# Performance work log

Measured on AMD Instinct MI355X. Metric: run time of the kernel, lower is better.

Reference implementation:

```python
import jax, jax.numpy as jnp
import numpy as np

C = 64            # x_channel (d_model)
D = 2 * C         # d_inner (expand=2)
N = C // 2        # d_state
K = 4             # scan directions
R = -(-C // 16)   # dt_rank = ceil(d_model/16)
Bsz, H, W = 2, 48, 48
EPS = 1e-5


def setup_inputs() -> dict:
    key = jax.random.key(0)
    ks = jax.random.split(key, 8)
    g = lambda k, shp, s: jax.random.normal(k, shp, dtype=jnp.float32) * s
    return {
        "fufea1": g(ks[0], (Bsz, C, H, W), 1.0),
        "ln_g": jnp.ones((C,), jnp.float32),
        "ln_b": jnp.zeros((C,), jnp.float32),
        "in_proj_w": g(ks[1], (2 * D, C), C ** -0.5),
        "conv_w": g(ks[2], (D, 1, 3, 3), 1.0 / 3.0),   # depthwise 3x3
        "conv_b": g(ks[3], (D,), 0.02),
        "x_proj_w": g(ks[4], (K, R + 2 * N, D), D ** -0.5),
        "dt_w": g(ks[5], (K, D, R), R ** -0.5),
        "dt_b": g(ks[6], (K, D), 0.1),
        "A_logs": jnp.log(jnp.tile(jnp.arange(1, N + 1, dtype=jnp.float32), (K, D, 1))),  # S4D-real init
        "Ds": jnp.ones((K, D), jnp.float32),
        "out_ln_g": jnp.ones((D,), jnp.float32),
        "out_ln_b": jnp.zeros((D,), jnp.float32),
        "out_proj_w": g(ks[7], (C, D), D ** -0.5),
    }


def _layernorm(x, g, b):
    mu = x.mean(-1, keepdims=True)
    var = ((x - mu) ** 2).mean(-1, keepdims=True)
    return (x - mu) * jax.lax.rsqrt(var + EPS) * g + b


def reference(fufea1, ln_g, ln_b, in_proj_w, conv_w, conv_b, x_proj_w,
              dt_w, dt_b, A_logs, Ds, out_ln_g, out_ln_b, out_proj_w):
    B, Cc, Hh, Ww = fufea1.shape
    L = Hh * Ww
    # pre-LN (over channels, channels-last)
    xn = _layernorm(fufea1.transpose(0, 2, 3, 1), ln_g, ln_b)          # (B,H,W,C)
    # SS2D: in_proj -> split x,z
    xz = xn @ in_proj_w.T                                               # (B,H,W,2D)
    x, z = jnp.split(xz, 2, axis=-1)
    x = x.transpose(0, 3, 1, 2)                                         # (B,D,H,W)
    x = jax.lax.conv_general_dilated(x, conv_w, (1, 1), "SAME",
                                     feature_group_count=D,
                                     dimension_numbers=("NCHW", "OIHW", "NCHW"))
    x = jax.nn.silu(x + conv_b[None, :, None, None])
    # 4-direction sequences: row-major, col-major, and their reverses
    x_hw = x.reshape(B, D, L)
    x_wh = x.transpose(0, 1, 3, 2).reshape(B, D, L)
    xs = jnp.stack([x_hw, x_wh], axis=1)                                # (B,2,D,L)
    xs = jnp.concatenate([xs, jnp.flip(xs, axis=-1)], axis=1)           # (B,K,D,L)
    # per-direction projections of dt, B, C
    x_dbl = jnp.einsum("bkdl,kcd->bkcl", xs, x_proj_w)
    dts, Bs, Cs = jnp.split(x_dbl, [R, R + N], axis=2)                  # (B,K,R,L),(B,K,N,L),(B,K,N,L)
    dts = jnp.einsum("bkrl,kdr->bkdl", dts, dt_w)
    delta = jax.nn.softplus(dts + dt_b[None, :, :, None])               # (B,K,D,L)
    A = -jnp.exp(A_logs)                                                # (K,D,N)
    # selective scan over L; carry h: (B,K,D,N)
    u_l = xs.transpose(3, 0, 1, 2)                                      # (L,B,K,D)
    dt_l = delta.transpose(3, 0, 1, 2)
    B_l = Bs.transpose(3, 0, 1, 2)                                      # (L,B,K,N)
    C_l = Cs.transpose(3, 0, 1, 2)

    def step(h, inp):
        u_t, d_t, b_t, c_t = inp
        dA = jnp.exp(d_t[..., None] * A)                                # (B,K,D,N)
        h = dA * h + (d_t * u_t)[..., None] * b_t[:, :, None, :]
        y = jnp.einsum("bkdn,bkn->bkd", h, c_t)
        return h, y

    h0 = jnp.zeros((B, K, D, N), xs.dtype)
    _, ys = jax.lax.scan(step, h0, (u_l, dt_l, B_l, C_l))               # ys: (L,B,K,D)
    out_y = ys.transpose(1, 2, 3, 0) + Ds[None, :, :, None] * xs        # (B,K,D,L)
    # merge the 4 directions back to row-major hw order
    inv_y = jnp.flip(out_y[:, 2:4], axis=-1)                            # (B,2,D,L)
    wh = lambda t: t.reshape(B, D, Ww, Hh).transpose(0, 1, 3, 2).reshape(B, D, L)
    y = out_y[:, 0] + inv_y[:, 0] + wh(out_y[:, 1]) + wh(inv_y[:, 1])   # (B,D,L)
    y = y.transpose(0, 2, 1).reshape(B, Hh, Ww, D)
    y = _layernorm(y, out_ln_g, out_ln_b) * jax.nn.silu(z)
    out = (y @ out_proj_w.T).transpose(0, 3, 1, 2) + fufea1             # residual add
    return out
```

## Files before the change

kernel.cpp:

```cpp
#include <hip/hip_runtime.h>

#define Cc 64
#define Dd 128
#define Nn 32
#define Kk 4
#define Rr 4
#define Bb 2
#define Hh 48
#define Ww 48
#define Ll 2304
#define EPSf 1e-5f
#define LCc 144

#if __has_builtin(__builtin_amdgcn_exp2f)
#define EXP2F __builtin_amdgcn_exp2f
#else
#define EXP2F exp2f
#endif

__device__ __forceinline__ float wsum64(float v) {
  v += __shfl_xor(v, 32);
  v += __shfl_xor(v, 16);
  v += __shfl_xor(v, 8);
  v += __shfl_xor(v, 4);
  v += __shfl_xor(v, 2);
  v += __shfl_xor(v, 1);
  return v;
}

__device__ __forceinline__ float hmax32(float v) {
  v = fmaxf(v, __shfl_xor(v, 1));
  v = fmaxf(v, __shfl_xor(v, 2));
  v = fmaxf(v, __shfl_xor(v, 4));
  v = fmaxf(v, __shfl_xor(v, 8));
  v = fmaxf(v, __shfl_xor(v, 16));
  return v;
}

__global__ __launch_bounds__(256) void k1_ln_inproj(
    const float* __restrict__ x, const float* __restrict__ g,
    const float* __restrict__ bta, const float* __restrict__ Wp,
    float* __restrict__ xin, float* __restrict__ zb)
{
  __shared__ float xS[16][65];
  __shared__ float xnS[16][64];
  const int tid = threadIdx.x;
  const int wv = tid >> 6, lane = tid & 63;
  const int pbase = blockIdx.x * 16;
  const int b = pbase / Ll;
  const int lbase = pbase % Ll;
  {
    const int c = tid >> 2, li0 = (tid & 3) * 4;
    const float4 v4 = *(const float4*)&x[(b * Cc + c) * Ll + lbase + li0];
    xS[li0 + 0][c] = v4.x;
    xS[li0 + 1][c] = v4.y;
    xS[li0 + 2][c] = v4.z;
    xS[li0 + 3][c] = v4.w;
  }
  __syncthreads();
  const float gv = g[lane], bv = bta[lane];
  for (int pi = 0; pi < 4; ++pi) {
    const int p = wv * 4 + pi;
    const float v = xS[p][lane];
    const float mu = wsum64(v) * (1.0f / 64.0f);
    const float dv = v - mu;
    const float var = wsum64(dv * dv) * (1.0f / 64.0f);
    const float rs = rsqrtf(var + EPSf);
    xnS[p][lane] = dv * rs * gv + bv;
  }
  __syncthreads();
  float acc[4][4];
  #pragma unroll
  for (int pi = 0; pi < 4; ++pi)
    #pragma unroll
    for (int m = 0; m < 4; ++m) acc[pi][m] = 0.f;
  const float4* W4 = (const float4*)Wp;
  #pragma unroll 4
  for (int c4 = 0; c4 < 16; ++c4) {
    float4 xn4[4];
    #pragma unroll
    for (int pi = 0; pi < 4; ++pi)
      xn4[pi] = ((const float4*)xnS[wv * 4 + pi])[c4];
    #pragma unroll
    for (int m = 0; m < 4; ++m) {
      const float4 w4 = W4[(lane + 64 * m) * 16 + c4];
      #pragma unroll
      for (int pi = 0; pi < 4; ++pi)
        acc[pi][m] += xn4[pi].x * w4.x + xn4[pi].y * w4.y +
                      xn4[pi].z * w4.z + xn4[pi].w * w4.w;
    }
  }
  #pragma unroll
  for (int pi = 0; pi < 4; ++pi) {
    const int l = lbase + wv * 4 + pi;
    const size_t base = (size_t)(b * Ll + l) * Dd;
    xin[base + lane]      = acc[pi][0];
    xin[base + lane + 64] = acc[pi][1];
    zb[base + lane]       = acc[pi][2];
    zb[base + lane + 64]  = acc[pi][3];
  }
}

__global__ __launch_bounds__(512) void k3_proj(
    const float* __restrict__ xin, const float* __restrict__ cw,
    const float* __restrict__ cb, const float* __restrict__ xpw,
    const float* __restrict__ dtw, const float* __restrict__ dtb,
    float* __restrict__ xc, float2* __restrict__ dd2,
    float* __restrict__ Bm, float* __restrict__ Cm)
{
  __shared__ float xinS[128][31];
  __shared__ float xvS[8][132];
  __shared__ float dtsS[8][16];
  const int t = threadIdx.x;
  const int pb = blockIdx.x * 8;
  const int b = pb / Ll;
  const int lb = pb % Ll;
  const int h0 = lb / Ww, w0 = lb % Ww;
  for (int i = t; i < 3840; i += 512) {
    const int d = i & 127, j = i >> 7;
    const int r = j / 10, c = j % 10;
    const int hh = h0 + r - 1, ww = w0 + c - 1;
    float v = 0.f;
    if (hh >= 0 && hh < Hh && ww >= 0 && ww < Ww)
      v = xin[((size_t)(b * Ll) + hh * Ww + ww) * Dd + d];
    xinS[d][j] = v;
  }
  __syncthreads();
  for (int i = t; i < 1024; i += 512) {
    const int pi = i >> 7, d = i & 127;
    float acc = cb[d];
    #pragma unroll
    for (int r = 0; r < 3; ++r)
      #pragma unroll
      for (int c = 0; c < 3; ++c)
        acc += xinS[d][r * 10 + pi + c] * cw[d * 9 + r * 3 + c];
    const float sig = 1.0f / (1.0f + __expf(-acc));
    xvS[pi][d] = acc * sig;
  }
  __syncthreads();
  if (t < 272) {
    const int k = t / 68, c = t % 68;
    const size_t bkL = (size_t)(b * Kk + k) * Ll;
    float acc[8];
    #pragma unroll
    for (int pi = 0; pi < 8; ++pi) acc[pi] = 0.f;
    const float4* w4p = (const float4*)(xpw + (k * 68 + c) * 128);
    for (int d4 = 0; d4 < 32; ++d4) {
      const float4 w4 = w4p[d4];
      #pragma unroll
      for (int pi = 0; pi < 8; ++pi) {
        const float4 x4 = ((const float4*)xvS[pi])[d4];
        acc[pi] += x4.x * w4.x + x4.y * w4.y + x4.z * w4.z + x4.w * w4.w;
      }
    }
    #pragma unroll
    for (int pi = 0; pi < 8; ++pi) {
      const int l0 = lb + pi;
      const int h = l0 / Ww, w = l0 % Ww;
      int lk;
      if      (k == 0) lk = l0;
      else if (k == 1) lk = w * Hh + h;
      else if (k == 2) lk = Ll - 1 - l0;
      else             lk = Ll - 1 - (w * Hh + h);
      if (c < Rr)            dtsS[pi][k * 4 + c] = acc[pi];
      else if (c < Rr + Nn)  Bm[(bkL + lk) * Nn + (c - Rr)] = acc[pi];
      else                   Cm[(bkL + lk) * Nn + (c - Rr - Nn)] = acc[pi];
    }
  } else {
    for (int i = t - 272; i < 1024; i += 240) {
      const int pi = i >> 7, d = i & 127;
      xc[((size_t)(b * Ll) + lb + pi) * Dd + d] = xvS[pi][d];
    }
  }
  __syncthreads();
  {
    const int k = t >> 7, dd = t & 127;
    const float4 dw = *(const float4*)&dtw[(k * Dd + dd) * 4];
    const float biasv = dtb[k * Dd + dd];
    float2* drow = dd2 + ((size_t)((b * Kk + k) * Dd) + dd) * Ll;
    float2 buf[8];
    #pragma unroll
    for (int pi = 0; pi < 8; ++pi) {
      const float a = biasv
          + dtsS[pi][k * 4 + 0] * dw.x + dtsS[pi][k * 4 + 1] * dw.y
          + dtsS[pi][k * 4 + 2] * dw.z + dtsS[pi][k * 4 + 3] * dw.w;
      const float sp = (a > 20.f) ? a : log1pf(__expf(a));
      buf[pi] = make_float2(sp, sp * xvS[pi][dd]);
    }
    if (k == 0) {
      float4* f4 = (float4*)(drow + lb);
      #pragma unroll
      for (int j = 0; j < 4; ++j)
        f4[j] = make_float4(buf[2 * j].x, buf[2 * j].y, buf[2 * j + 1].x, buf[2 * j + 1].y);
    } else if (k == 2) {
      float4* f4 = (float4*)(drow + (Ll - 8 - lb));
      #pragma unroll
      for (int j = 0; j < 4; ++j)
        f4[j] = make_float4(buf[7 - 2 * j].x, buf[7 - 2 * j].y, buf[6 - 2 * j].x, buf[6 - 2 * j].y);
    } else {
      #pragma unroll
      for (int pi = 0; pi < 8; ++pi) {
        const int l0 = lb + pi;
        const int h = l0 / Ww, w = l0 % Ww;
        int lk = w * Hh + h;
        if (k == 3) lk = Ll - 1 - lk;
        drow[lk] = buf[pi];
      }
    }
  }
}

__global__ __launch_bounds__(512) void k4_scan(
    const float2* __restrict__ dd2, const float* __restrict__ Bm,
    const float* __restrict__ Cm, const float* __restrict__ Alogs,
    float* __restrict__ ys)
{
  __shared__ float hendS[16][32];
  __shared__ float carryS[16][32];
  __shared__ float sumDS[16];
  __shared__ float cmaxS[16];
  __shared__ float pS[16][8][36];
  const int tid = threadIdx.x;
  const int s = tid >> 5, n = tid & 31;
  const int blk = blockIdx.x;
  const int bk = blk & 7;
  const int d = blk >> 3;
  const int b = bk >> 2, k = bk & 3;
  const float An = -__expf(Alogs[(k * Dd + d) * Nn + n]);
  const float AnE = An * 1.44269504f;
  const size_t bkL = (size_t)(b * Kk + k) * Ll;
  const float2* dP = dd2 + ((size_t)((b * Kk + k) * Dd) + d) * Ll;
  const float* bP = Bm + bkL * Nn + n;
  const float* cP = Cm + bkL * Nn + n;
  const int lbeg = s * LCc;
  float* yP = ys + ((size_t)((b * Kk + k) * Dd) + d) * Ll + lbeg;
  const int rrow = n & 7, qtr = n >> 3;

  float h = 0.f, sumD = 0.f, cmx = 0.f;
  {
    const float4* q4 = (const float4*)(dP + lbeg);
    const float* bl = bP + (size_t)lbeg * Nn;
    const float* cl = cP + (size_t)lbeg * Nn;
    float4 qa = q4[0], qb = q4[1];
    float b0 = bl[0], b1 = bl[Nn], b2 = bl[2 * Nn], b3 = bl[3 * Nn];
    float c0 = cl[0], c1 = cl[Nn], c2 = cl[2 * Nn], c3 = cl[3 * Nn];
    for (int t8 = 0; t8 < LCc / 8; ++t8) {
      #pragma unroll
      for (int half = 0; half < 2; ++half) {
        q4 += 2; bl += 4 * Nn; cl += 4 * Nn;
        const float4 qa_n = q4[0], qb_n = q4[1];
        const float b0n = bl[0], b1n = bl[Nn], b2n = bl[2 * Nn], b3n = bl[3 * Nn];
        const float c0n = cl[0], c1n = cl[Nn], c2n = cl[2 * Nn], c3n = cl[3 * Nn];
        h = EXP2F(qa.x * AnE) * h + qa.y * b0; pS[s][half * 4 + 0][n] = h * c0;
        h = EXP2F(qa.z * AnE) * h + qa.w * b1; pS[s][half * 4 + 1][n] = h * c1;
        h = EXP2F(qb.x * AnE) * h + qb.y * b2; pS[s][half * 4 + 2][n] = h * c2;
        h = EXP2F(qb.z * AnE) * h + qb.w * b3; pS[s][half * 4 + 3][n] = h * c3;
        sumD += (qa.x + qa.z) + (qb.x + qb.z);
        cmx = fmaxf(cmx, fmaxf(fmaxf(fabsf(c0), fabsf(c1)),
                               fmaxf(fabsf(c2), fabsf(c3))));
        qa = qa_n; qb = qb_n; b0 = b0n; b1 = b1n; b2 = b2n; b3 = b3n;
        c0 = c0n; c1 = c1n; c2 = c2n; c3 = c3n;
      }
      const float4 a4 = *(const float4*)&pS[s][rrow][qtr * 8];
      const float4 d4v = *(const float4*)&pS[s][rrow][qtr * 8 + 4];
      float sum = ((a4.x + a4.y) + (a4.z + a4.w)) + ((d4v.x + d4v.y) + (d4v.z + d4v.w));
      sum += __shfl_xor(sum, 8);
      sum += __shfl_xor(sum, 16);
      if (n < 8) yP[t8 * 8 + n] = sum;
    }
  }
  hendS[s][n] = h;
  const float cmxAll = hmax32(cmx);
  if (n == 0) { sumDS[s] = sumD; cmaxS[s] = cmxAll; }
  __syncthreads();
  if (tid < 32) {
    float carry = 0.f;
    #pragma unroll
    for (int s2 = 0; s2 < 16; ++s2) {
      carryS[s2][tid] = carry;
      carry = EXP2F(AnE * sumDS[s2]) * carry + hendS[s2][tid];
    }
  }
  __syncthreads();
  const float carry = carryS[s][n];
  const float mc = hmax32(fabsf(carry));
  const float AmaxE = hmax32(AnE);
  const float Pstop = log2f(mc * cmaxS[s] * 3.2e6f) / (-AmaxE);
  {
    float hc = carry, P = 0.f;
    const float4* q4 = (const float4*)(dP + lbeg);
    const float* cl = cP + (size_t)lbeg * Nn;
    for (int t8 = 0; t8 < LCc / 8; ++t8) {
      if (!(P < Pstop)) break;
      #pragma unroll
      for (int half = 0; half < 2; ++half) {
        const float4 qa = q4[0], qb = q4[1];
        q4 += 2;
        hc *= EXP2F(qa.x * AnE); pS[s][half * 4 + 0][n] = hc * cl[0];
        hc *= EXP2F(qa.z * AnE); pS[s][half * 4 + 1][n] = hc * cl[Nn];
        hc *= EXP2F(qb.x * AnE); pS[s][half * 4 + 2][n] = hc * cl[2 * Nn];
        hc *= EXP2F(qb.z * AnE); pS[s][half * 4 + 3][n] = hc * cl[3 * Nn];
        P += (qa.x + qa.z) + (qb.x + qb.z);
        cl += 4 * Nn;
      }
      const float4 a4 = *(const float4*)&pS[s][rrow][qtr * 8];
      const float4 d4v = *(const float4*)&pS[s][rrow][qtr * 8 + 4];
      float sum = ((a4.x + a4.y) + (a4.z + a4.w)) + ((d4v.x + d4v.y) + (d4v.z + d4v.w));
      sum += __shfl_xor(sum, 8);
      sum += __shfl_xor(sum, 16);
      if (n < 8) yP[t8 * 8 + n] += sum;
    }
  }
}

__global__ __launch_bounds__(256) void k5_merge(
    const float* __restrict__ ys, const float* __restrict__ zb,
    const float* __restrict__ og, const float* __restrict__ ob,
    const float* __restrict__ Wo, const float* __restrict__ resid,
    const float* __restrict__ xc, const float* __restrict__ DsP,
    float* __restrict__ out)
{
  __shared__ float ysS[4][16][128];
  __shared__ float tS[16][128];
  __shared__ float oS[64][17];
  __shared__ float xcS[16][128];
  const int tid = threadIdx.x;
  const int wv = tid >> 6, lane = tid & 63;
  const int tb = blockIdx.x;
  const int b = tb / 144;
  const int ti = tb % 144;
  const int tr = ti / 12, tc = ti % 12;
  const int h0 = tr * 4, w0 = tc * 4;
  {
    const int p = tid >> 4, qq = tid & 15;
    const int l0 = (h0 + (p >> 2)) * Ww + w0 + (p & 3);
    const float4* src = (const float4*)&xc[((size_t)(b * Ll) + l0) * Dd];
    ((float4*)xcS[p])[qq]      = src[qq];
    ((float4*)xcS[p])[qq + 16] = src[qq + 16];
  }
  {
    const int dch = tid & 127, half = tid >> 7;
    #pragma unroll
    for (int ii = 0; ii < 2; ++ii) {
      const int i = half * 2 + ii;
      const int l0 = (h0 + i) * Ww + w0;
      float4 v;
      v = *(const float4*)&ys[((size_t)(b * Kk + 0) * Dd + dch) * Ll + l0];
      ysS[0][i * 4 + 0][dch] = v.x; ysS[0][i * 4 + 1][dch] = v.y;
      ysS[0][i * 4 + 2][dch] = v.z; ysS[0][i * 4 + 3][dch] = v.w;
      const int r2 = Ll - 4 - (h0 + i) * Ww - w0;
      v = *(const float4*)&ys[((size_t)(b * Kk + 2) * Dd + dch) * Ll + r2];
      ysS[2][i * 4 + 3][dch] = v.x; ysS[2][i * 4 + 2][dch] = v.y;
      ysS[2][i * 4 + 1][dch] = v.z; ysS[2][i * 4 + 0][dch] = v.w;
    }
    #pragma unroll
    for (int jj = 0; jj < 2; ++jj) {
      const int j = half * 2 + jj;
      const int l1 = (w0 + j) * Hh + h0;
      float4 v = *(const float4*)&ys[((size_t)(b * Kk + 1) * Dd + dch) * Ll + l1];
      ysS[1][0 * 4 + j][dch] = v.x; ysS[1][1 * 4 + j][dch] = v.y;
      ysS[1][2 * 4 + j][dch] = v.z; ysS[1][3 * 4 + j][dch] = v.w;
      const int r3 = Ll - 4 - (w0 + j) * Hh - h0;
      v = *(const float4*)&ys[((size_t)(b * Kk + 3) * Dd + dch) * Ll + r3];
      ysS[3][3 * 4 + j][dch] = v.x; ysS[3][2 * 4 + j][dch] = v.y;
      ysS[3][1 * 4 + j][dch] = v.z; ysS[3][0 * 4 + j][dch] = v.w;
    }
  }
  float sDs[2];
  #pragma unroll
  for (int m = 0; m < 2; ++m) {
    const int dch = lane + 64 * m;
    sDs[m] = DsP[dch] + DsP[Dd + dch] + DsP[2 * Dd + dch] + DsP[3 * Dd + dch];
  }
  __syncthreads();
  for (int pi = 0; pi < 4; ++pi) {
    const int p = wv * 4 + pi;
    const int l0 = (h0 + (p >> 2)) * Ww + w0 + (p & 3);
    float tv[2];
    #pragma unroll
    for (int m = 0; m < 2; ++m) {
      const int dch = lane + 64 * m;
      tv[m] = ysS[0][p][dch] + ysS[1][p][dch] + ysS[2][p][dch] + ysS[3][p][dch]
            + sDs[m] * xcS[p][dch];
    }
    const float mu = wsum64(tv[0] + tv[1]) * (1.0f / 128.0f);
    const float q = wsum64((tv[0] - mu) * (tv[0] - mu) +
                           (tv[1] - mu) * (tv[1] - mu)) * (1.0f / 128.0f);
    const float rs = rsqrtf(q + EPSf);
    #pragma unroll
    for (int m = 0; m < 2; ++m) {
      const int dch = lane + 64 * m;
      const float zz = zb[(size_t)(b * Ll + l0) * Dd + dch];
      const float sig = 1.0f / (1.0f + __expf(-zz));
      tS[p][dch] = ((tv[m] - mu) * rs * og[dch] + ob[dch]) * (zz * sig);
    }
  }
  __syncthreads();
  float acc[4] = {0.f, 0.f, 0.f, 0.f};
  const float4* W4 = (const float4*)Wo;
  for (int d4 = 0; d4 < 32; ++d4) {
    const float4 w4 = W4[lane * 32 + d4];
    #pragma unroll
    for (int pi = 0; pi < 4; ++pi) {
      const float4 t4 = ((const float4*)tS[wv * 4 + pi])[d4];
      acc[pi] += t4.x * w4.x + t4.y * w4.y + t4.z * w4.z + t4.w * w4.w;
    }
  }
  #pragma unroll
  for (int pi = 0; pi < 4; ++pi) oS[lane][wv * 4 + pi] = acc[pi];
  __syncthreads();
  const int c = tid >> 2, q = tid & 3;
  const size_t obase = (size_t)(b * Cc + c) * Ll + (size_t)(h0 + q) * Ww + w0;
  const float4 r4 = *(const float4*)(resid + obase);
  float4 o4;
  o4.x = oS[c][q * 4 + 0] + r4.x;
  o4.y = oS[c][q * 4 + 1] + r4.y;
  o4.z = oS[c][q * 4 + 2] + r4.z;
  o4.w = oS[c][q * 4 + 3] + r4.w;
  *(float4*)(out + obase) = o4;
}

extern "C" void kernel_launch(void* const* d_in, const int* in_sizes, int n_in,
                              void* d_out, int out_size, void* d_ws, size_t ws_size,
                              hipStream_t stream)
{
  (void)in_sizes; (void)n_in; (void)out_size; (void)ws_size;
  const float* fufea1     = (const float*)d_in[0];
  const float* ln_g       = (const float*)d_in[1];
  const float* ln_b       = (const float*)d_in[2];
  const float* in_proj_w  = (const float*)d_in[3];
  const float* conv_w     = (const float*)d_in[4];
  const float* conv_b     = (const float*)d_in[5];
  const float* x_proj_w   = (const float*)d_in[6];
  const float* dt_w       = (const float*)d_in[7];
  const float* dt_b       = (const float*)d_in[8];
  const float* A_logs     = (const float*)d_in[9];
  const float* Ds         = (const float*)d_in[10];
  const float* out_ln_g   = (const float*)d_in[11];
  const float* out_ln_b   = (const float*)d_in[12];
  const float* out_proj_w = (const float*)d_in[13];

  float* ws = (float*)d_ws;
  float2* dd2 = (float2*)ws;
  float* Bm   = ws + 4718592;
  float* Cm   = ws + 5308416;
  float* zb   = ws + 5898240;
  float* xc   = ws + 6488064;
  float* ysb  = ws + 7077888;
  float* xin  = ws + 7077888;

  k1_ln_inproj<<<288, 256, 0, stream>>>(fufea1, ln_g, ln_b, in_proj_w, xin, zb);
  k3_proj<<<576, 512, 0, stream>>>(xin, conv_w, conv_b, x_proj_w, dt_w, dt_b,
                                   xc, dd2, Bm, Cm);
  k4_scan<<<1024, 512, 0, stream>>>(dd2, Bm, Cm, A_logs, ysb);
  k5_merge<<<288, 256, 0, stream>>>(ysb, zb, out_ln_g, out_ln_b, out_proj_w, fufea1,
                                    xc, Ds, (float*)d_out);
}
```

Measured before the change: 201.0 us.

## Write scan outputs directly in row-major pixel order and simplify merge loads

```diff
diff --git a/kernel.cpp b/kernel.cpp
--- a/kernel.cpp
+++ b/kernel.cpp
@@ -233,7 +233,8 @@
   const float* bP = Bm + bkL * Nn + n;
   const float* cP = Cm + bkL * Nn + n;
   const int lbeg = s * LCc;
-  float* yP = ys + ((size_t)((b * Kk + k) * Dd) + d) * Ll + lbeg;
+  float* yD = ys + ((size_t)((b * Kk + k) * Dd) + d) * Ll;
+  const int pstr = (k == 0) ? 1 : (k == 1) ? Ww : (k == 2) ? -1 : -Ww;
   const int rrow = n & 7, qtr = n >> 3;
 
   float h = 0.f, sumD = 0.f, cmx = 0.f;
@@ -266,7 +267,15 @@
       float sum = ((a4.x + a4.y) + (a4.z + a4.w)) + ((d4v.x + d4v.y) + (d4v.z + d4v.w));
       sum += __shfl_xor(sum, 8);
       sum += __shfl_xor(sum, 16);
-      if (n < 8) yP[t8 * 8 + n] = sum;
+      if (n < 8) {
+        const int j0 = lbeg + t8 * 8;
+        int pb0;
+        if      (k == 0) pb0 = j0;
+        else if (k == 2) pb0 = Ll - 1 - j0;
+        else if (k == 1) pb0 = (j0 % Hh) * Ww + (j0 / Hh);
+        else { const int jr = Ll - 1 - j0; pb0 = (jr % Hh) * Ww + (jr / Hh); }
+        yD[pb0 + n * pstr] = sum;
+      }
     }
   }
   hendS[s][n] = h;
@@ -308,7 +317,15 @@
       float sum = ((a4.x + a4.y) + (a4.z + a4.w)) + ((d4v.x + d4v.y) + (d4v.z + d4v.w));
       sum += __shfl_xor(sum, 8);
       sum += __shfl_xor(sum, 16);
-      if (n < 8) yP[t8 * 8 + n] += sum;
+      if (n < 8) {
+        const int j0 = lbeg + t8 * 8;
+        int pb0;
+        if      (k == 0) pb0 = j0;
+        else if (k == 2) pb0 = Ll - 1 - j0;
+        else if (k == 1) pb0 = (j0 % Hh) * Ww + (j0 / Hh);
+        else { const int jr = Ll - 1 - j0; pb0 = (jr % Hh) * Ww + (jr / Hh); }
+        yD[pb0 + n * pstr] += sum;
+      }
     }
   }
 }
@@ -320,51 +337,33 @@
     const float* __restrict__ xc, const float* __restrict__ DsP,
     float* __restrict__ out)
 {
-  __shared__ float ysS[4][16][128];
+  __shared__ float ysS[4][16][132];
+  __shared__ float xcS[16][128];
   __shared__ float tS[16][128];
   __shared__ float oS[64][17];
-  __shared__ float xcS[16][128];
   const int tid = threadIdx.x;
   const int wv = tid >> 6, lane = tid & 63;
-  const int tb = blockIdx.x;
-  const int b = tb / 144;
-  const int ti = tb % 144;
-  const int tr = ti / 12, tc = ti % 12;
-  const int h0 = tr * 4, w0 = tc * 4;
-  {
-    const int p = tid >> 4, qq = tid & 15;
-    const int l0 = (h0 + (p >> 2)) * Ww + w0 + (p & 3);
-    const float4* src = (const float4*)&xc[((size_t)(b * Ll) + l0) * Dd];
-    ((float4*)xcS[p])[qq]      = src[qq];
-    ((float4*)xcS[p])[qq + 16] = src[qq + 16];
-  }
-  {
-    const int dch = tid & 127, half = tid >> 7;
-    #pragma unroll
-    for (int ii = 0; ii < 2; ++ii) {
-      const int i = half * 2 + ii;
-      const int l0 = (h0 + i) * Ww + w0;
-      float4 v;
-      v = *(const float4*)&ys[((size_t)(b * Kk + 0) * Dd + dch) * Ll + l0];
-      ysS[0][i * 4 + 0][dch] = v.x; ysS[0][i * 4 + 1][dch] = v.y;
-      ysS[0][i * 4 + 2][dch] = v.z; ysS[0][i * 4 + 3][dch] = v.w;
-      const int r2 = Ll - 4 - (h0 + i) * Ww - w0;
-      v = *(const float4*)&ys[((size_t)(b * Kk + 2) * Dd + dch) * Ll + r2];
-      ysS[2][i * 4 + 3][dch] = v.x; ysS[2][i * 4 + 2][dch] = v.y;
-      ysS[2][i * 4 + 1][dch] = v.z; ysS[2][i * 4 + 0][dch] = v.w;
-    }
-    #pragma unroll
-    for (int jj = 0; jj < 2; ++jj) {
-      const int j = half * 2 + jj;
-      const int l1 = (w0 + j) * Hh + h0;
-      float4 v = *(const float4*)&ys[((size_t)(b * Kk + 1) * Dd + dch) * Ll + l1];
-      ysS[1][0 * 4 + j][dch] = v.x; ysS[1][1 * 4 + j][dch] = v.y;
-      ysS[1][2 * 4 + j][dch] = v.z; ysS[1][3 * 4 + j][dch] = v.w;
-      const int r3 = Ll - 4 - (w0 + j) * Hh - h0;
-      v = *(const float4*)&ys[((size_t)(b * Kk + 3) * Dd + dch) * Ll + r3];
-      ysS[3][3 * 4 + j][dch] = v.x; ysS[3][2 * 4 + j][dch] = v.y;
-      ysS[3][1 * 4 + j][dch] = v.z; ysS[3][0 * 4 + j][dch] = v.w;
-    }
+  const int pbase = blockIdx.x * 16;
+  const int b = pbase / Ll;
+  const int lbase = pbase % Ll;
+  {
+    const int li0 = (tid & 3) * 4, dh = tid >> 2;
+    #pragma unroll
+    for (int it = 0; it < 2; ++it) {
+      const int d = dh + 64 * it;
+      #pragma unroll
+      for (int k = 0; k < 4; ++k) {
+        const float4 v = *(const float4*)&ys[((size_t)(b * Kk + k) * Dd + d) * Ll + lbase + li0];
+        ysS[k][li0 + 0][d] = v.x; ysS[k][li0 + 1][d] = v.y;
+        ysS[k][li0 + 2][d] = v.z; ysS[k][li0 + 3][d] = v.w;
+      }
+    }
+  }
+  {
+    const int p = tid >> 4, q = tid & 15;
+    const float4* src = (const float4*)&xc[((size_t)(b * Ll) + lbase + p) * Dd];
+    ((float4*)xcS[p])[q]      = src[q];
+    ((float4*)xcS[p])[q + 16] = src[q + 16];
   }
   float sDs[2];
   #pragma unroll
@@ -375,7 +374,7 @@
   __syncthreads();
   for (int pi = 0; pi < 4; ++pi) {
     const int p = wv * 4 + pi;
-    const int l0 = (h0 + (p >> 2)) * Ww + w0 + (p & 3);
+    const int l0 = lbase + p;
     float tv[2];
     #pragma unroll
     for (int m = 0; m < 2; ++m) {
@@ -409,14 +408,14 @@
   #pragma unroll
   for (int pi = 0; pi < 4; ++pi) oS[lane][wv * 4 + pi] = acc[pi];
   __syncthreads();
-  const int c = tid >> 2, q = tid & 3;
-  const size_t obase = (size_t)(b * Cc + c) * Ll + (size_t)(h0 + q) * Ww + w0;
+  const int c = tid >> 2, off = (tid & 3) * 4;
+  const size_t obase = (size_t)(b * Cc + c) * Ll + lbase + off;
   const float4 r4 = *(const float4*)(resid + obase);
   float4 o4;
-  o4.x = oS[c][q * 4 + 0] + r4.x;
-  o4.y = oS[c][q * 4 + 1] + r4.y;
-  o4.z = oS[c][q * 4 + 2] + r4.z;
-  o4.w = oS[c][q * 4 + 3] + r4.w;
+  o4.x = oS[c][off + 0] + r4.x;
+  o4.y = oS[c][off + 1] + r4.y;
+  o4.z = oS[c][off + 2] + r4.z;
+  o4.w = oS[c][off + 3] + r4.w;
   *(float4*)(out + obase) = o4;
 }
 
```

Result: no change. 201.5 us (+0.2%).
